# Kernel tuning notes

Measured on AMD Instinct MI355X. Metric: run time of the kernel, lower is better.

Reference implementation:

```python
import jax, jax.numpy as jnp
import numpy as np
import math

B, T, D, WINDOW, VOCAB = 16, 2048, 128, 16, 42
EPS = 1e-5


def setup_inputs() -> dict:
    key = jax.random.key(0)
    ks = jax.random.split(key, 16)
    def lin(k, fan_in, fan_out):
        bound = 1.0 / math.sqrt(fan_in)
        kw, kb = jax.random.split(k)
        w = jax.random.uniform(kw, (fan_in, fan_out), minval=-bound, maxval=bound, dtype=jnp.float32)
        b = jax.random.uniform(kb, (fan_out,), minval=-bound, maxval=bound, dtype=jnp.float32)
        return w, b
    emb = jax.random.normal(ks[0], (VOCAB, D), dtype=jnp.float32)
    w1, b1 = lin(ks[1], 2 * D, D // 2)
    w2, b2 = lin(ks[2], D // 2, 1)
    wv_w, wv_b = lin(ks[3], D, D)
    mg_w, mg_b = lin(ks[4], 2 * D, D)
    ln_g = jnp.ones((D,), jnp.float32)
    ln_b = jnp.zeros((D,), jnp.float32)
    head_w, head_b = lin(ks[5], D, VOCAB)
    input_ids = jax.random.randint(ks[6], (B, T), 0, VOCAB, dtype=jnp.int64 if jax.config.jax_enable_x64 else jnp.int32)
    return {"input_ids": input_ids, "emb": emb, "w1": w1, "b1": b1, "w2": w2, "b2": b2,
            "wv_w": wv_w, "wv_b": wv_b, "mg_w": mg_w, "mg_b": mg_b,
            "ln_g": ln_g, "ln_b": ln_b, "head_w": head_w, "head_b": head_b}


def _build_neighbors(x):
    # nb[:, t, w] = x[:, t - w - 1] if t >= w + 1 else 0  (vectorized shift-by-(w+1))
    Tlen = x.shape[1]
    nbs = [jnp.pad(x[:, : Tlen - (w + 1)], ((0, 0), (w + 1, 0), (0, 0))) for w in range(WINDOW)]
    return jnp.stack(nbs, axis=2)  # [B, T, WINDOW, D]


def reference(input_ids, emb, w1, b1, w2, b2, wv_w, wv_b, mg_w, mg_b, ln_g, ln_b, head_w, head_b):
    x = emb[input_ids]                      # [B, T, D]
    Tlen = x.shape[1]
    nb = _build_neighbors(x)                # [B, T, W, D]
    h_t = jnp.broadcast_to(x[:, :, None, :], nb.shape)
    pair = jnp.concatenate([h_t, nb], axis=-1)            # [B, T, W, 2D]
    hid = jax.nn.silu(pair @ w1 + b1)                      # [B, T, W, D//2]
    tau = jax.nn.sigmoid((hid @ w2 + b2)[..., 0])          # [B, T, W]
    v = nb @ wv_w + wv_b                                   # [B, T, W, D]
    msg = jnp.einsum('btw,btwd->btd', tau, v)              # [B, T, D]
    y = jnp.concatenate([x, msg], axis=-1) @ mg_w + mg_b   # [B, T, D]
    mu = jnp.mean(y, axis=-1, keepdims=True)
    var = jnp.mean(jnp.square(y - mu), axis=-1, keepdims=True)
    y = (y - mu) * jax.lax.rsqrt(var + EPS) * ln_g + ln_b
    omega = 2.0 * math.pi / 12.0
    phase = Tlen * omega                                   # timestep = input_ids.shape[1]
    scale = 1.0 + 0.15 * jnp.sin(jnp.arange(Tlen, dtype=jnp.float32) * omega + phase)
    y = y * scale[None, :, None]
    return y @ head_w + head_b                             # [B, T, VOCAB]
```

## Files before the change

kernel.cpp:

```cpp
#include <hip/hip_runtime.h>
#include <hip/hip_bf16.h>
#include <math.h>

typedef __attribute__((ext_vector_type(8))) short short8;
typedef __attribute__((ext_vector_type(4))) float f32x4;

#define T_SEQ 2048
#define NVOC 42

#define OFF_UE  0
#define OFF_RE  2688
#define OFF_VE  5376
#define OFF_TAU 10880
#define OFF_WB  12688
#define OFF_HB  18832

static __device__ __forceinline__ short f2b(float x){
  __hip_bfloat16 h = __float2bfloat16(x);
  return *reinterpret_cast<short*>(&h);
}

__global__ __launch_bounds__(256) void k_pre1(const float* __restrict__ emb,
    const float* __restrict__ w1, const float* __restrict__ b1,
    const float* __restrict__ wv_w, const float* __restrict__ wv_b,
    const float* __restrict__ mg_w, const float* __restrict__ mg_b,
    const float* __restrict__ head_w, float* __restrict__ ws){
  __shared__ __align__(16) float s_e[128];
  __shared__ __align__(16) float s_p[256];
  int blk = blockIdx.x, tid = threadIdx.x;
  ushort* wbu = (ushort*)(ws + OFF_WB);
  if (blk < 127){
    int mode = (blk < 42) ? 0 : ((blk < 85) ? 1 : 2);
    int row  = (mode == 0) ? blk : ((mode == 1) ? blk - 42 : blk - 85);
    bool pad = (mode == 1 && row == 42);
    if (tid < 128) s_e[tid] = pad ? 0.f : emb[row*128 + tid];
    __syncthreads();
    int o = tid & 127, h = tid >> 7;
    float acc = 0.f;
    if (mode == 0){
      int col = o & 63;
      const float* wp = w1 + ((o < 64) ? 0 : 128*64) + (h*64)*64 + col;
      const float* ep = s_e + h*64;
      #pragma unroll
      for (int chunk = 0; chunk < 4; ++chunk){
        float wreg[16];
        #pragma unroll
        for (int j = 0; j < 16; ++j) wreg[j] = wp[(chunk*16 + j)*64];
        #pragma unroll
        for (int j = 0; j < 16; ++j) acc = fmaf(ep[chunk*16 + j], wreg[j], acc);
      }
    } else {
      const float* wm = (mode == 1) ? wv_w : mg_w;
      const float* wp = wm + (h*64)*128 + o;
      const float* ep = s_e + h*64;
      #pragma unroll
      for (int chunk = 0; chunk < 4; ++chunk){
        float wreg[16];
        #pragma unroll
        for (int j = 0; j < 16; ++j) wreg[j] = wp[(chunk*16 + j)*128];
        #pragma unroll
        for (int j = 0; j < 16; ++j) acc = fmaf(ep[chunk*16 + j], wreg[j], acc);
      }
    }
    s_p[h*128 + o] = acc;
    __syncthreads();
    if (h == 0){
      float v = s_p[o] + s_p[128 + o];
      if (mode == 0){
        if (o < 64) ws[OFF_UE + row*64 + o] = v + b1[o];
        else        ws[OFF_RE + row*64 + (o - 64)] = v;
      } else if (mode == 1){
        ws[OFF_VE + row*128 + o] = v + wv_b[o];
      } else {
        float ya = v + mg_b[o];
        int d = o, k = 43 + row;
        wbu[(((d>>4)*3 + (k>>5))*64 + (((k>>3)&3)*16 + (d&15)))*8 + (k&7)] = (ushort)f2b(ya);
      }
    }
  } else {
    ushort* hbu = (ushort*)(ws + OFF_HB);
    for (int i2 = tid; i2 < 6144; i2 += 256){
      int f = i2 >> 9, ln = (i2 >> 3) & 63, j = i2 & 7;
      int n2 = f >> 2, cc = f & 3;
      int k = cc*32 + (ln>>4)*8 + j;
      int col = n2*16 + (ln & 15);
      float v = (col < NVOC) ? head_w[k*NVOC + col] : 0.f;
      hbu[i2] = (ushort)f2b(v);
    }
    for (int i = tid; i < 1408; i += 256){
      int n = i/176, rem = i%176, k = 85 + rem/16, col = rem%16;
      wbu[((n*3 + 2)*64 + (((k>>3)&3)*16 + col))*8 + (k&7)] = 0;
    }
  }
}

__global__ __launch_bounds__(256) void k_pre2(const float* __restrict__ w2,
    const float* __restrict__ b2, const float* __restrict__ mg_w,
    float* __restrict__ ws){
  __shared__ __align__(16) float s_v[128];
  __shared__ __align__(16) float s_p[256];
  int blk = blockIdx.x, tid = threadIdx.x;
  ushort* wbu = (ushort*)(ws + OFF_WB);
  if (blk < 42){
    int a = blk;
    if (tid < 64) s_v[tid] = ws[OFF_UE + a*64 + tid];
    __syncthreads();
    int o = tid & 63, h = tid >> 6;
    float part = 0.f;
    if (o < 43){
      float rreg[16], wreg[16];
      #pragma unroll
      for (int j = 0; j < 16; ++j){
        int k = h*16 + j;
        rreg[j] = (o < 42) ? ws[OFF_RE + o*64 + k] : 0.f;
        wreg[j] = w2[k];
      }
      #pragma unroll
      for (int j = 0; j < 16; ++j){
        float hh = s_v[h*16 + j] + rreg[j];
        float sg = 1.f/(1.f + __expf(-hh));
        part = fmaf(hh*sg, wreg[j], part);
      }
    }
    s_p[h*64 + o] = part;
    __syncthreads();
    if (h == 0 && o < 43){
      float s = s_p[o] + s_p[64+o] + s_p[128+o] + s_p[192+o] + b2[0];
      ws[OFF_TAU + a*43 + o] = 1.f/(1.f + __expf(-s));
    }
  } else {
    int c = blk - 42;
    if (tid < 128) s_v[tid] = ws[OFF_VE + c*128 + tid];
    __syncthreads();
    int o = tid & 127, h = tid >> 7;
    const float* wp = mg_w + (128 + h*64)*128 + o;
    const float* vp = s_v + h*64;
    float acc = 0.f;
    #pragma unroll
    for (int chunk = 0; chunk < 4; ++chunk){
      float wreg[16];
      #pragma unroll
      for (int j = 0; j < 16; ++j) wreg[j] = wp[(chunk*16 + j)*128];
      #pragma unroll
      for (int j = 0; j < 16; ++j) acc = fmaf(vp[chunk*16 + j], wreg[j], acc);
    }
    s_p[h*128 + o] = acc;
    __syncthreads();
    if (h == 0){
      float vm = s_p[o] + s_p[128 + o];
      int d = o, k = c;
      wbu[(((d>>4)*3 + (k>>5))*64 + (((k>>3)&3)*16 + (d&15)))*8 + (k&7)] = (ushort)f2b(vm);
    }
  }
}

__global__ __launch_bounds__(256) void k_main(const int* __restrict__ ids,
    const float* __restrict__ ln_g, const float* __restrict__ ln_b,
    const float* __restrict__ head_b, const float* __restrict__ ws,
    float* __restrict__ out){
  __shared__ __align__(16) float s_T[4][1600];
  int tid = threadIdx.x, wv = tid >> 6, lane = tid & 63;
  int r = lane & 15, q = lane >> 4;
  int base = blockIdx.x*64 + wv*16;
  const ushort* wbu = (const ushort*)(ws + OFF_WB);

  int l32 = lane & 31;
  int idv = NVOC;
  if (!(((base & (T_SEQ-1)) == 0) && (l32 < 16))) idv = ids[base - 16 + l32];

  short8 HBf[3][4];
  {
    const ushort* hbsrc = (const ushort*)(ws + OFF_HB);
    #pragma unroll
    for (int n2 = 0; n2 < 3; ++n2)
      #pragma unroll
      for (int c = 0; c < 4; ++c)
        HBf[n2][c] = *(const short8*)&hbsrc[((n2*4 + c)*64 + lane)*8];
  }
  float gd[8], bd[8];
  #pragma unroll
  for (int n = 0; n < 8; ++n){ gd[n] = ln_g[n*16 + r]; bd[n] = ln_b[n*16 + r]; }
  float hb3[3];
  #pragma unroll
  for (int n2 = 0; n2 < 3; ++n2){ int col = n2*16 + r; hb3[n2] = (col < NVOC) ? head_b[col] : 0.f; }

  float* T = s_T[wv];
  {
    float4 z; z.x=z.y=z.z=z.w=0.f;
    float4* t4 = (float4*)T;
    #pragma unroll
    for (int i = 0; i < 7; ++i){ int idx = lane + i*64; if (idx < 400) t4[idx] = z; }
  }
  int a = __shfl(idv, 16 + r);
  const float* tau_g = ws + OFF_TAU;
  #pragma unroll
  for (int m = 0; m < 4; ++m){
    int w = q*4 + m;
    int c = __shfl(idv, r + 15 - w);
    float tv = tau_g[a*43 + c];
    atomicAdd(&T[r*100 + c], tv);
  }
  if (q == 0) T[r*100 + 43 + a] = 1.0f;
  __asm__ volatile("s_waitcnt lgkmcnt(0)" ::: "memory");

  short8 A1[3];
  #pragma unroll
  for (int ct = 0; ct < 3; ++ct){
    const float4* p = (const float4*)&T[r*100 + ct*32 + q*8];
    float4 u0 = p[0], u1 = p[1];
    short8 v;
    v[0]=f2b(u0.x); v[1]=f2b(u0.y); v[2]=f2b(u0.z); v[3]=f2b(u0.w);
    v[4]=f2b(u1.x); v[5]=f2b(u1.y); v[6]=f2b(u1.z); v[7]=f2b(u1.w);
    A1[ct] = v;
  }

  f32x4 accm[8];
  #pragma unroll
  for (int n = 0; n < 8; ++n){ accm[n][0]=0.f; accm[n][1]=0.f; accm[n][2]=0.f; accm[n][3]=0.f; }
  #pragma unroll
  for (int ct = 0; ct < 3; ++ct){
    #pragma unroll
    for (int n = 0; n < 8; ++n){
      short8 b = *(const short8*)&wbu[((n*3 + ct)*64 + lane)*8];
      accm[n] = __builtin_amdgcn_mfma_f32_16x16x32_bf16(A1[ct], b, accm[n], 0, 0, 0);
    }
  }

  ushort* sY = (ushort*)T;
  #pragma unroll
  for (int reg = 0; reg < 4; ++reg){
    float s1 = 0.f, s2 = 0.f;
    #pragma unroll
    for (int n = 0; n < 8; ++n){ float y = accm[n][reg]; s1 += y; s2 = fmaf(y, y, s2); }
    #pragma unroll
    for (int mk = 1; mk < 16; mk <<= 1){ s1 += __shfl_xor(s1, mk); s2 += __shfl_xor(s2, mk); }
    float mu  = s1 * (1.f/128.f);
    float var = s2 * (1.f/128.f) - mu*mu;
    float rinv = rsqrtf(var + 1e-5f);
    int tok = base + q*4 + reg;
    int m12 = ((tok & (T_SEQ-1)) + 8) % 12;
    float sc = fmaf(0.15f, __sinf((float)m12 * 0.52359877559829887f), 1.0f);
    float A_ = rinv * sc;
    #pragma unroll
    for (int n = 0; n < 8; ++n){
      float yl = (accm[n][reg] - mu) * A_;
      float o  = fmaf(yl, gd[n], bd[n]*sc);
      sY[(q*4 + reg)*136 + n*16 + r] = (ushort)f2b(o);
    }
  }

  f32x4 acch[3];
  #pragma unroll
  for (int n2 = 0; n2 < 3; ++n2){ acch[n2][0]=0.f; acch[n2][1]=0.f; acch[n2][2]=0.f; acch[n2][3]=0.f; }
  short8 A2[4];
  #pragma unroll
  for (int c = 0; c < 4; ++c)
    A2[c] = *(const short8*)&sY[r*136 + c*32 + q*8];
  #pragma unroll
  for (int c = 0; c < 4; ++c){
    #pragma unroll
    for (int n2 = 0; n2 < 3; ++n2)
      acch[n2] = __builtin_amdgcn_mfma_f32_16x16x32_bf16(A2[c], HBf[n2][c], acch[n2], 0, 0, 0);
  }
  #pragma unroll
  for (int n2 = 0; n2 < 3; ++n2){
    int col = n2*16 + r;
    if (col < NVOC){
      #pragma unroll
      for (int reg = 0; reg < 4; ++reg){
        int tok = base + q*4 + reg;
        out[tok*NVOC + col] = acch[n2][reg] + hb3[n2];
      }
    }
  }
}

extern "C" void kernel_launch(void* const* d_in, const int* in_sizes, int n_in,
                              void* d_out, int out_size, void* d_ws, size_t ws_size,
                              hipStream_t stream){
  const int*   ids    = (const int*)  d_in[0];
  const float* emb    = (const float*)d_in[1];
  const float* w1     = (const float*)d_in[2];
  const float* b1     = (const float*)d_in[3];
  const float* w2     = (const float*)d_in[4];
  const float* b2     = (const float*)d_in[5];
  const float* wv_w   = (const float*)d_in[6];
  const float* wv_b   = (const float*)d_in[7];
  const float* mg_w   = (const float*)d_in[8];
  const float* mg_b   = (const float*)d_in[9];
  const float* ln_g   = (const float*)d_in[10];
  const float* ln_b   = (const float*)d_in[11];
  const float* head_w = (const float*)d_in[12];
  const float* head_b = (const float*)d_in[13];
  float* ws  = (float*)d_ws;
  float* out = (float*)d_out;
  k_pre1<<<dim3(128), dim3(256), 0, stream>>>(emb, w1, b1, wv_w, wv_b, mg_w, mg_b,
                                              head_w, ws);
  k_pre2<<<dim3(85),  dim3(256), 0, stream>>>(w2, b2, mg_w, ws);
  k_main<<<dim3(512), dim3(256), 0, stream>>>(ids, ln_g, ln_b, head_b, ws, out);
}
```

Measured before the change: 22.95 us.

## Merge two precompute kernels into one, computing tau and value projections per block

Fuses the two preprocessing kernels into a single launch. Blocks that previously wrote intermediate UE/RE/VE tables now compute tau directly: each block loads all embeddings into shared memory, recomputes the neighbour projections, and reduces across the wave with shuffles. The value rows get their msg-side mg_w projection within the same block. This removes a kernel launch and the global round trip of intermediates, at the cost of redundant recomputation of the neighbour projection in each of the 42 tau blocks and a larger shared-memory footprint.

```diff
diff --git a/kernel.cpp b/kernel.cpp
--- a/kernel.cpp
+++ b/kernel.cpp
@@ -8,73 +8,153 @@
 #define T_SEQ 2048
 #define NVOC 42
 
-#define OFF_UE  0
-#define OFF_RE  2688
-#define OFF_VE  5376
-#define OFF_TAU 10880
-#define OFF_WB  12688
-#define OFF_HB  18832
+#define OFF_TAU 0
+#define OFF_WB  1808
+#define OFF_HB  7952
 
 static __device__ __forceinline__ short f2b(float x){
   __hip_bfloat16 h = __float2bfloat16(x);
   return *reinterpret_cast<short*>(&h);
 }
 
-__global__ __launch_bounds__(256) void k_pre1(const float* __restrict__ emb,
+__global__ __launch_bounds__(256) void k_pre(const float* __restrict__ emb,
     const float* __restrict__ w1, const float* __restrict__ b1,
+    const float* __restrict__ w2, const float* __restrict__ b2,
     const float* __restrict__ wv_w, const float* __restrict__ wv_b,
     const float* __restrict__ mg_w, const float* __restrict__ mg_b,
     const float* __restrict__ head_w, float* __restrict__ ws){
-  __shared__ __align__(16) float s_e[128];
-  __shared__ __align__(16) float s_p[256];
+  __shared__ __align__(16) float sm[5376];
   int blk = blockIdx.x, tid = threadIdx.x;
   ushort* wbu = (ushort*)(ws + OFF_WB);
-  if (blk < 127){
-    int mode = (blk < 42) ? 0 : ((blk < 85) ? 1 : 2);
-    int row  = (mode == 0) ? blk : ((mode == 1) ? blk - 42 : blk - 85);
-    bool pad = (mode == 1 && row == 42);
+  if (blk < 42){
+    int a = blk;
+    {
+      float4* d4 = (float4*)sm;
+      const float4* e4 = (const float4*)emb;
+      for (int i = tid; i < 1344; i += 256) d4[i] = e4[i];
+    }
+    int lane = tid & 63;
+    int wvu = __builtin_amdgcn_readfirstlane(tid >> 6);
+    int k = lane;
+    float w2k = w2[k];
+    float uacc = b1[k];
+    float b20 = b2[0];
+    __syncthreads();
+    float reacc[11];
+    #pragma unroll
+    for (int cc = 0; cc < 11; ++cc) reacc[cc] = 0.f;
+
+    float wuA[16], wrA[16], wuB[16], wrB[16];
+    auto LOADW = [&](int ch, float* wu, float* wr){
+      #pragma unroll
+      for (int j = 0; j < 16; ++j){
+        wu[j] = w1[(ch*16 + j)*64 + k];
+        wr[j] = w1[(128 + ch*16 + j)*64 + k];
+      }
+    };
+    auto COMPUTE = [&](int ch, const float* wu, const float* wr){
+      {
+        const float4* ea = (const float4*)(sm + a*128 + ch*16);
+        #pragma unroll
+        for (int t = 0; t < 4; ++t){
+          float4 e = ea[t];
+          uacc = fmaf(e.x, wu[t*4+0], uacc);
+          uacc = fmaf(e.y, wu[t*4+1], uacc);
+          uacc = fmaf(e.z, wu[t*4+2], uacc);
+          uacc = fmaf(e.w, wu[t*4+3], uacc);
+        }
+      }
+      #pragma unroll
+      for (int cc = 0; cc < 11; ++cc){
+        int c = wvu + 4*cc;
+        if (c < 42){
+          const float4* ec = (const float4*)(sm + c*128 + ch*16);
+          #pragma unroll
+          for (int t = 0; t < 4; ++t){
+            float4 e = ec[t];
+            reacc[cc] = fmaf(e.x, wr[t*4+0], reacc[cc]);
+            reacc[cc] = fmaf(e.y, wr[t*4+1], reacc[cc]);
+            reacc[cc] = fmaf(e.z, wr[t*4+2], reacc[cc]);
+            reacc[cc] = fmaf(e.w, wr[t*4+3], reacc[cc]);
+          }
+        }
+      }
+    };
+    LOADW(0, wuA, wrA);
+    #pragma unroll
+    for (int ch2 = 0; ch2 < 4; ++ch2){
+      LOADW(2*ch2+1, wuB, wrB);
+      COMPUTE(2*ch2, wuA, wrA);
+      if (ch2 < 3) LOADW(2*ch2+2, wuA, wrA);
+      COMPUTE(2*ch2+1, wuB, wrB);
+    }
+    #pragma unroll
+    for (int cc = 0; cc < 11; ++cc){
+      int c = wvu + 4*cc;
+      if (c < 43){
+        float h  = uacc + ((c < 42) ? reacc[cc] : 0.f);
+        float sg = 1.f/(1.f + __expf(-h));
+        float sl = h * sg * w2k;
+        #pragma unroll
+        for (int mk = 1; mk < 64; mk <<= 1) sl += __shfl_xor(sl, mk);
+        if (lane == 0)
+          ws[OFF_TAU + a*43 + c] = 1.f/(1.f + __expf(-(sl + b20)));
+      }
+    }
+  } else if (blk < 127){
+    bool isC = (blk < 85);
+    int row = isC ? (blk - 42) : (blk - 85);
+    float* s_e  = sm;
+    float* s_p  = sm + 128;
+    float* s_ve = sm + 384;
+    bool pad = (isC && row == 42);
     if (tid < 128) s_e[tid] = pad ? 0.f : emb[row*128 + tid];
     __syncthreads();
     int o = tid & 127, h = tid >> 7;
-    float acc = 0.f;
-    if (mode == 0){
-      int col = o & 63;
-      const float* wp = w1 + ((o < 64) ? 0 : 128*64) + (h*64)*64 + col;
+    {
+      const float* wm = isC ? wv_w : mg_w;
+      const float* wp = wm + (h*64)*128 + o;
       const float* ep = s_e + h*64;
+      float acc = 0.f;
       #pragma unroll
       for (int chunk = 0; chunk < 4; ++chunk){
         float wreg[16];
         #pragma unroll
-        for (int j = 0; j < 16; ++j) wreg[j] = wp[(chunk*16 + j)*64];
+        for (int j = 0; j < 16; ++j) wreg[j] = wp[(chunk*16 + j)*128];
         #pragma unroll
         for (int j = 0; j < 16; ++j) acc = fmaf(ep[chunk*16 + j], wreg[j], acc);
       }
-    } else {
-      const float* wm = (mode == 1) ? wv_w : mg_w;
-      const float* wp = wm + (h*64)*128 + o;
-      const float* ep = s_e + h*64;
-      #pragma unroll
-      for (int chunk = 0; chunk < 4; ++chunk){
-        float wreg[16];
-        #pragma unroll
-        for (int j = 0; j < 16; ++j) wreg[j] = wp[(chunk*16 + j)*128];
-        #pragma unroll
-        for (int j = 0; j < 16; ++j) acc = fmaf(ep[chunk*16 + j], wreg[j], acc);
-      }
-    }
-    s_p[h*128 + o] = acc;
+      s_p[h*128 + o] = acc;
+    }
     __syncthreads();
-    if (h == 0){
-      float v = s_p[o] + s_p[128 + o];
-      if (mode == 0){
-        if (o < 64) ws[OFF_UE + row*64 + o] = v + b1[o];
-        else        ws[OFF_RE + row*64 + (o - 64)] = v;
-      } else if (mode == 1){
-        ws[OFF_VE + row*128 + o] = v + wv_b[o];
-      } else {
-        float ya = v + mg_b[o];
+    if (!isC){
+      if (h == 0){
+        float ya = s_p[o] + s_p[128 + o] + mg_b[o];
         int d = o, k = 43 + row;
         wbu[(((d>>4)*3 + (k>>5))*64 + (((k>>3)&3)*16 + (d&15)))*8 + (k&7)] = (ushort)f2b(ya);
+      }
+    } else {
+      if (h == 0) s_ve[o] = s_p[o] + s_p[128 + o] + wv_b[o];
+      __syncthreads();
+      {
+        const float* wp = mg_w + (128 + h*64)*128 + o;
+        const float* vp = s_ve + h*64;
+        float acc = 0.f;
+        #pragma unroll
+        for (int chunk = 0; chunk < 4; ++chunk){
+          float wreg[16];
+          #pragma unroll
+          for (int j = 0; j < 16; ++j) wreg[j] = wp[(chunk*16 + j)*128];
+          #pragma unroll
+          for (int j = 0; j < 16; ++j) acc = fmaf(vp[chunk*16 + j], wreg[j], acc);
+        }
+        s_p[h*128 + o] = acc;
+      }
+      __syncthreads();
+      if (h == 0){
+        float vm = s_p[o] + s_p[128 + o];
+        int d = o, k = row;
+        wbu[(((d>>4)*3 + (k>>5))*64 + (((k>>3)&3)*16 + (d&15)))*8 + (k&7)] = (ushort)f2b(vm);
       }
     }
   } else {
@@ -90,66 +170,6 @@
     for (int i = tid; i < 1408; i += 256){
       int n = i/176, rem = i%176, k = 85 + rem/16, col = rem%16;
       wbu[((n*3 + 2)*64 + (((k>>3)&3)*16 + col))*8 + (k&7)] = 0;
-    }
-  }
-}
-
-__global__ __launch_bounds__(256) void k_pre2(const float* __restrict__ w2,
-    const float* __restrict__ b2, const float* __restrict__ mg_w,
-    float* __restrict__ ws){
-  __shared__ __align__(16) float s_v[128];
-  __shared__ __align__(16) float s_p[256];
-  int blk = blockIdx.x, tid = threadIdx.x;
-  ushort* wbu = (ushort*)(ws + OFF_WB);
-  if (blk < 42){
-    int a = blk;
-    if (tid < 64) s_v[tid] = ws[OFF_UE + a*64 + tid];
-    __syncthreads();
-    int o = tid & 63, h = tid >> 6;
-    float part = 0.f;
-    if (o < 43){
-      float rreg[16], wreg[16];
-      #pragma unroll
-      for (int j = 0; j < 16; ++j){
-        int k = h*16 + j;
-        rreg[j] = (o < 42) ? ws[OFF_RE + o*64 + k] : 0.f;
-        wreg[j] = w2[k];
-      }
-      #pragma unroll
-      for (int j = 0; j < 16; ++j){
-        float hh = s_v[h*16 + j] + rreg[j];
-        float sg = 1.f/(1.f + __expf(-hh));
-        part = fmaf(hh*sg, wreg[j], part);
-      }
-    }
-    s_p[h*64 + o] = part;
-    __syncthreads();
-    if (h == 0 && o < 43){
-      float s = s_p[o] + s_p[64+o] + s_p[128+o] + s_p[192+o] + b2[0];
-      ws[OFF_TAU + a*43 + o] = 1.f/(1.f + __expf(-s));
-    }
-  } else {
-    int c = blk - 42;
-    if (tid < 128) s_v[tid] = ws[OFF_VE + c*128 + tid];
-    __syncthreads();
-    int o = tid & 127, h = tid >> 7;
-    const float* wp = mg_w + (128 + h*64)*128 + o;
-    const float* vp = s_v + h*64;
-    float acc = 0.f;
-    #pragma unroll
-    for (int chunk = 0; chunk < 4; ++chunk){
-      float wreg[16];
-      #pragma unroll
-      for (int j = 0; j < 16; ++j) wreg[j] = wp[(chunk*16 + j)*128];
-      #pragma unroll
-      for (int j = 0; j < 16; ++j) acc = fmaf(vp[chunk*16 + j], wreg[j], acc);
-    }
-    s_p[h*128 + o] = acc;
-    __syncthreads();
-    if (h == 0){
-      float vm = s_p[o] + s_p[128 + o];
-      int d = o, k = c;
-      wbu[(((d>>4)*3 + (k>>5))*64 + (((k>>3)&3)*16 + (d&15)))*8 + (k&7)] = (ushort)f2b(vm);
     }
   }
 }
@@ -294,8 +314,7 @@
   const float* head_b = (const float*)d_in[13];
   float* ws  = (float*)d_ws;
   float* out = (float*)d_out;
-  k_pre1<<<dim3(128), dim3(256), 0, stream>>>(emb, w1, b1, wv_w, wv_b, mg_w, mg_b,
-                                              head_w, ws);
-  k_pre2<<<dim3(85),  dim3(256), 0, stream>>>(w2, b2, mg_w, ws);
+  k_pre <<<dim3(128), dim3(256), 0, stream>>>(emb, w1, b1, w2, b2, wv_w, wv_b,
+                                              mg_w, mg_b, head_w, ws);
   k_main<<<dim3(512), dim3(256), 0, stream>>>(ids, ln_g, ln_b, head_b, ws, out);
 }
```

Measured after the change: 30.20 us. 31.6% more time.
